# Optimization experiments

Hardware: AMD Instinct MI355X
Metric: run time of the kernel (lower is better)

Reference implementation:

```python
import jax, jax.numpy as jnp
import numpy as np

B, S, HID = 2, 2048, 2048
NK, NV, DK, DV, K = 16, 32, 128, 128, 4
KEY_DIM = NK * DK          # 2048
VAL_DIM = NV * DV          # 4096
CONV_DIM = 2 * KEY_DIM + VAL_DIM  # 8192
EPS = 1e-6


def setup_inputs() -> dict:
    key = jax.random.key(0)
    ks = jax.random.split(key, 8)
    n = lambda k, shape, sc: jax.random.normal(k, shape, jnp.float32) * sc
    return {
        "hidden_states": n(ks[0], (B, S, HID), 1.0),
        "W_qkv": n(ks[1], (CONV_DIM, HID), 0.02),
        "W_z": n(ks[2], (VAL_DIM, HID), 0.02),
        "W_b": n(ks[3], (NV, HID), 0.02),
        "W_a": n(ks[4], (NV, HID), 0.02),
        "conv_w": n(ks[5], (CONV_DIM, K), 0.3),   # depthwise conv weight, squeeze(1) of [C,1,K]
        "norm_w": jnp.ones((DV,), jnp.float32),
        "W_out": n(ks[6], (HID, VAL_DIM), 0.02),
        "dt_bias": jnp.ones((NV,), jnp.float32),
        "A_log": jnp.zeros((NV,), jnp.float32),
    }


def _l2norm(t):
    return t * jax.lax.rsqrt(jnp.sum(t * t, axis=-1, keepdims=True) + EPS)


def _forward(hidden_states, W_qkv, W_z, W_b, W_a, conv_w, norm_w, W_out, dt_bias, A_log):
    b_, s_, _ = hidden_states.shape
    mixed = hidden_states @ W_qkv.T                     # [B,S,CONV_DIM]
    z = (hidden_states @ W_z.T).reshape(b_, s_, NV, DV)  # gate branch
    b_proj = hidden_states @ W_b.T                      # [B,S,NV]
    a_proj = hidden_states @ W_a.T                      # [B,S,NV]

    # causal depthwise conv1d (groups=CONV_DIM, no bias) + silu
    x = jnp.transpose(mixed, (0, 2, 1))                 # [B,C,S]
    x = jnp.pad(x, ((0, 0), (0, 0), (K - 1, 0)))
    x = jax.lax.conv_general_dilated(
        x, conv_w[:, None, :], window_strides=(1,), padding="VALID",
        feature_group_count=CONV_DIM)
    mixed = jnp.transpose(jax.nn.silu(x), (0, 2, 1))    # [B,S,CONV_DIM]

    q, k, v = jnp.split(mixed, [KEY_DIM, 2 * KEY_DIM], axis=-1)
    q = q.reshape(b_, s_, NK, DK)
    k = k.reshape(b_, s_, NK, DK)
    v = v.reshape(b_, s_, NV, DV)

    beta = jax.nn.sigmoid(b_proj)                                    # [B,S,NV]
    g = -jnp.exp(A_log) * jax.nn.softplus(a_proj + dt_bias)          # [B,S,NV], log decay

    rep = NV // NK
    q = jnp.repeat(q, rep, axis=2)                      # GQA expand -> [B,S,NV,DK]
    k = jnp.repeat(k, rep, axis=2)
    q = _l2norm(q)
    k = _l2norm(k)
    scale = DK ** -0.5

    def step(state, inp):  # state: [B,NV,DK,DV]
        qt, kt, vt, gt, bt = inp  # [B,NV,DK],[B,NV,DK],[B,NV,DV],[B,NV],[B,NV]
        state = state * jnp.exp(gt)[..., None, None]
        mem = jnp.einsum('bhk,bhkv->bhv', kt, state)
        delta = (vt - mem) * bt[..., None]
        state = state + jnp.einsum('bhk,bhv->bhkv', kt, delta)
        ot = jnp.einsum('bhk,bhkv->bhv', qt * scale, state)
        return state, ot

    init = jnp.zeros((b_, NV, DK, DV), jnp.float32)
    xs = (jnp.moveaxis(q, 1, 0), jnp.moveaxis(k, 1, 0), jnp.moveaxis(v, 1, 0),
          jnp.moveaxis(g, 1, 0), jnp.moveaxis(beta, 1, 0))
    _, o = jax.lax.scan(step, init, xs)                 # [S,B,NV,DV]
    o = jnp.moveaxis(o, 0, 1)                           # [B,S,NV,DV]

    # RMSNormGated over head_v_dim, then silu(z) gate
    var = jnp.mean(o * o, axis=-1, keepdims=True)
    o = o * jax.lax.rsqrt(var + EPS) * norm_w
    o = (o * jax.nn.silu(z)).reshape(b_, s_, VAL_DIM)
    return o @ W_out.T


def reference(hidden_states, W_qkv, W_z, W_b, W_a, conv_w, norm_w, W_out, dt_bias, A_log):
    return _forward(hidden_states, W_qkv, W_z, W_b, W_a, conv_w, norm_w, W_out, dt_bias, A_log)
```

## Files before the change

kernel.cpp:

```cpp
#include <hip/hip_runtime.h>
#include <hip/hip_bf16.h>
#include <math.h>

#define DEVI __device__ __forceinline__

typedef __attribute__((ext_vector_type(4))) float f32x4;
typedef __attribute__((ext_vector_type(8))) short s16x8;
typedef __attribute__((ext_vector_type(4))) unsigned int u32x4;

DEVI float bf2f(ushort u){ union{unsigned int i; float f;} x; x.i = ((unsigned int)u)<<16; return x.f; }
DEVI ushort f2bf(float f){ union{float f; unsigned int i;} x; x.f = f;
  unsigned int r = x.i + 0x7fffu + ((x.i>>16)&1u); return (ushort)(r>>16); }

#define MFMA16(a,b,c) __builtin_amdgcn_mfma_f32_16x16x32_bf16(a,b,c,0,0,0)

__global__ __launch_bounds__(256) void cvt_bf16(const float* __restrict__ in, ushort* __restrict__ out){
  int i = blockIdx.x*256 + threadIdx.x;
  float4 v = ((const float4*)in)[i];
  ushort4 o; o.x = f2bf(v.x); o.y = f2bf(v.y); o.z = f2bf(v.z); o.w = f2bf(v.w);
  ((ushort4*)out)[i] = o;
}

DEVI void gl_lds16(const ushort* g, ushort* l){
  __builtin_amdgcn_global_load_lds((const __attribute__((address_space(1))) void*)g,
                                   (__attribute__((address_space(3))) void*)l, 16, 0, 0);
}

#define SBAR() __builtin_amdgcn_s_barrier()
#define LGKM0() do{ asm volatile("s_waitcnt lgkmcnt(0)" ::: "memory"); __builtin_amdgcn_sched_barrier(0); }while(0)
#define VMC6() asm volatile("s_waitcnt vmcnt(6)" ::: "memory")
#define VMC4() asm volatile("s_waitcnt vmcnt(4)" ::: "memory")

template<int BF16_OUT>
__global__ __launch_bounds__(512, 2) void gemm256(const ushort* __restrict__ A,
                                                  const ushort* __restrict__ B,
                                                  void* __restrict__ Cv,
                                                  int M, int N, int K,
                                                  int rpx, int cpx){
  __shared__ ushort smem[65536];
  __shared__ ushort dummy[4096];
  const int tid = threadIdx.x, w = tid>>6, lane = tid&63;
  const int fr = lane&15, quad = lane>>4;
  const int wm = w>>2, wn = w&3;
  const int NT = K>>6;

  const int nbn = N>>8;
  const int bid = blockIdx.x;
  const int xcd = bid & 7, idx = bid >> 3;
  const int CGn = nbn / cpx;
  const int rgrp = xcd / CGn, cgrp = xcd % CGn;
  const int rloc = idx % rpx, cloc = idx / rpx;
  const long tileM = (long)(rgrp*rpx + rloc) << 8;
  const long tileN = (long)(cgrp*cpx + cloc) << 8;

  const int rr  = (tid&63)>>2;
  const int cc  = ((tid&3)*8) ^ ((rr&8)?16:0);
  const int row0 = (w>>1)*16 + rr;
  const int col0 = (w&1)*32 + cc;
  const long off0 = (long)row0*K + col0;
  const long h64 = 64l*K;

  const ushort* pA0 = A + tileM*K + off0;
  const ushort* pA1 = pA0 + 128l*K;
  const ushort* pB0 = B + tileN*K + off0;
  const ushort* pB1 = pB0 + 128l*K;

  const int dw = w*512;
  ushort* dmy = dummy + dw;

#define ST_A0(bb,tt) do{ if((tt)<NT){ const long kk=(long)(tt)<<6; \
    gl_lds16(pA0+kk, smem+(bb)*32768+dw);        gl_lds16(pA1+kk, smem+(bb)*32768+8192+dw);} \
    else { gl_lds16(pA0, dmy); gl_lds16(pA1, dmy);} }while(0)
#define ST_A1(bb,tt) do{ if((tt)<NT){ const long kk=((long)(tt)<<6)+h64; \
    gl_lds16(pA0+kk, smem+(bb)*32768+4096+dw);   gl_lds16(pA1+kk, smem+(bb)*32768+12288+dw);} \
    else { gl_lds16(pA0, dmy); gl_lds16(pA1, dmy);} }while(0)
#define ST_B0(bb,tt) do{ if((tt)<NT){ const long kk=(long)(tt)<<6; \
    gl_lds16(pB0+kk, smem+(bb)*32768+16384+dw);  gl_lds16(pB1+kk, smem+(bb)*32768+24576+dw);} \
    else { gl_lds16(pB0, dmy); gl_lds16(pB1, dmy);} }while(0)
#define ST_B1(bb,tt) do{ if((tt)<NT){ const long kk=((long)(tt)<<6)+h64; \
    gl_lds16(pB0+kk, smem+(bb)*32768+20480+dw);  gl_lds16(pB1+kk, smem+(bb)*32768+28672+dw);} \
    else { gl_lds16(pB0, dmy); gl_lds16(pB1, dmy);} }while(0)

  const int baseF = fr*32 + ((quad*8) ^ ((fr&8)?16:0));
  const int sB = (wn&1)*4;

  f32x4 acc[8][4];
  #pragma unroll
  for (int i=0;i<8;i++)
    #pragma unroll
    for (int j=0;j<4;j++) acc[i][j] = (f32x4){0.f,0.f,0.f,0.f};

  ST_A0(0,0); ST_B0(0,0); ST_B1(0,0); ST_A1(0,0);
  ST_A0(1,1); ST_B0(1,1); ST_B1(1,1);
  VMC6();
  SBAR();

  #pragma unroll 2
  for (int t=0; t<NT; ++t){
    const int bs = t&1;
    const ushort* SA = smem + bs*32768 + wm*8192;
    const ushort* SB = smem + bs*32768 + 16384 + (wn>>1)*8192;
    s16x8 af[4][2], bl[2][2], bh[2][2];
    #pragma unroll
    for (int mt=0;mt<4;mt++)
      #pragma unroll
      for (int ks=0;ks<2;ks++)
        af[mt][ks] = *(const s16x8*)(SA + ((mt*2+ks)<<9) + baseF);
    #pragma unroll
    for (int nt=0;nt<2;nt++)
      #pragma unroll
      for (int ks=0;ks<2;ks++)
        bl[nt][ks] = *(const s16x8*)(SB + (((sB+nt)*2+ks)<<9) + baseF);
    ST_A1(bs^1, t+1);
    SBAR(); LGKM0();
    __builtin_amdgcn_s_setprio(1);
    #pragma unroll
    for (int mt=0;mt<4;mt++)
      #pragma unroll
      for (int nt=0;nt<2;nt++){
        acc[mt][nt] = MFMA16(af[mt][0], bl[nt][0], acc[mt][nt]);
        acc[mt][nt] = MFMA16(af[mt][1], bl[nt][1], acc[mt][nt]);
      }
    __builtin_amdgcn_s_setprio(0);
    SBAR();
    #pragma unroll
    for (int nt=0;nt<2;nt++)
      #pragma unroll
      for (int ks=0;ks<2;ks++)
        bh[nt][ks] = *(const s16x8*)(SB + (((sB+2+nt)*2+ks)<<9) + baseF);
    ST_A0(bs, t+2);
    SBAR(); LGKM0();
    __builtin_amdgcn_s_setprio(1);
    #pragma unroll
    for (int mt=0;mt<4;mt++)
      #pragma unroll
      for (int nt=0;nt<2;nt++){
        acc[mt][2+nt] = MFMA16(af[mt][0], bh[nt][0], acc[mt][2+nt]);
        acc[mt][2+nt] = MFMA16(af[mt][1], bh[nt][1], acc[mt][2+nt]);
      }
    __builtin_amdgcn_s_setprio(0);
    SBAR();
    #pragma unroll
    for (int mt=0;mt<4;mt++)
      #pragma unroll
      for (int ks=0;ks<2;ks++)
        af[mt][ks] = *(const s16x8*)(SA + (((4+mt)*2+ks)<<9) + baseF);
    ST_B0(bs, t+2);
    SBAR(); LGKM0();
    __builtin_amdgcn_s_setprio(1);
    #pragma unroll
    for (int mt=0;mt<4;mt++)
      #pragma unroll
      for (int nt=0;nt<2;nt++){
        acc[4+mt][nt] = MFMA16(af[mt][0], bl[nt][0], acc[4+mt][nt]);
        acc[4+mt][nt] = MFMA16(af[mt][1], bl[nt][1], acc[4+mt][nt]);
      }
    __builtin_amdgcn_s_setprio(0);
    SBAR();
    ST_B1(bs, t+2);
    SBAR();
    __builtin_amdgcn_s_setprio(1);
    #pragma unroll
    for (int mt=0;mt<4;mt++)
      #pragma unroll
      for (int nt=0;nt<2;nt++){
        acc[4+mt][2+nt] = MFMA16(af[mt][0], bh[nt][0], acc[4+mt][2+nt]);
        acc[4+mt][2+nt] = MFMA16(af[mt][1], bh[nt][1], acc[4+mt][2+nt]);
      }
    __builtin_amdgcn_s_setprio(0);
    VMC6();
    SBAR();
  }
#undef ST_A0
#undef ST_A1
#undef ST_B0
#undef ST_B1

  const long Rb = tileM + wm*128 + quad*4;
  const long Cb = tileN + wn*64 + fr;
  if (BF16_OUT){
    ushort* C = (ushort*)Cv;
    #pragma unroll
    for (int mt=0;mt<8;mt++)
      #pragma unroll
      for (int r=0;r<4;r++){
        const long row = Rb + mt*16 + r;
        #pragma unroll
        for (int nt=0;nt<4;nt++)
          C[row*(long)N + Cb + nt*16] = f2bf(acc[mt][nt][r]);
      }
  } else {
    float* C = (float*)Cv;
    #pragma unroll
    for (int mt=0;mt<8;mt++)
      #pragma unroll
      for (int r=0;r<4;r++){
        const long row = Rb + mt*16 + r;
        #pragma unroll
        for (int nt=0;nt<4;nt++)
          C[row*(long)N + Cb + nt*16] = acc[mt][nt][r];
      }
  }
}

template<int BF16_OUT>
__global__ __launch_bounds__(512, 2) void gemm256n128(const ushort* __restrict__ A,
                                                      const ushort* __restrict__ B,
                                                      void* __restrict__ Cv,
                                                      int M, int N, int K,
                                                      int rpx, int cpx){
  __shared__ ushort smem[49152];
  __shared__ ushort dummy[4096];
  const int tid = threadIdx.x, w = tid>>6, lane = tid&63;
  const int fr = lane&15, quad = lane>>4;
  const int wm = w>>2, wn = w&3;
  const int NT = K>>6;

  const int nbn = N>>7;
  const int bid = blockIdx.x;
  const int xcd = bid & 7, idx = bid >> 3;
  const int CGn = nbn / cpx;
  const int rgrp = xcd / CGn, cgrp = xcd % CGn;
  const int rloc = idx % rpx, cloc = idx / rpx;
  const long tileM = (long)(rgrp*rpx + rloc) << 8;
  const long tileN = (long)(cgrp*cpx + cloc) << 7;

  const int rr  = (tid&63)>>2;
  const int cc  = ((tid&3)*8) ^ ((rr&8)?16:0);
  const int row0 = (w>>1)*16 + rr;
  const int col0 = (w&1)*32 + cc;
  const long off0 = (long)row0*K + col0;
  const long h64 = 64l*K;

  const ushort* pA0 = A + tileM*K + off0;
  const ushort* pA1 = pA0 + 128l*K;
  const ushort* pB0 = B + tileN*K + off0;

  const int dw = w*512;
  ushort* dmy = dummy + dw;

#define ST_A0(bb,tt) do{ if((tt)<NT){ const long kk=(long)(tt)<<6; \
    gl_lds16(pA0+kk, smem+(bb)*24576+dw);        gl_lds16(pA1+kk, smem+(bb)*24576+8192+dw);} \
    else { gl_lds16(pA0, dmy); gl_lds16(pA1, dmy);} }while(0)
#define ST_A1(bb,tt) do{ if((tt)<NT){ const long kk=((long)(tt)<<6)+h64; \
    gl_lds16(pA0+kk, smem+(bb)*24576+4096+dw);   gl_lds16(pA1+kk, smem+(bb)*24576+12288+dw);} \
    else { gl_lds16(pA0, dmy); gl_lds16(pA1, dmy);} }while(0)
#define ST_B(bb,tt) do{ if((tt)<NT){ const long kk=(long)(tt)<<6; \
    gl_lds16(pB0+kk, smem+(bb)*24576+16384+dw);  gl_lds16(pB0+kk+h64, smem+(bb)*24576+20480+dw);} \
    else { gl_lds16(pB0, dmy); gl_lds16(pB0, dmy);} }while(0)

  const int baseF = fr*32 + ((quad*8) ^ ((fr&8)?16:0));

  f32x4 acc[8][2];
  #pragma unroll
  for (int i=0;i<8;i++)
    #pragma unroll
    for (int j=0;j<2;j++) acc[i][j] = (f32x4){0.f,0.f,0.f,0.f};

  ST_A0(0,0); ST_B(0,0); ST_A1(0,0);
  ST_A0(1,1); ST_B(1,1);
  VMC4();
  SBAR();

  #pragma unroll 2
  for (int t=0; t<NT; ++t){
    const int bs = t&1;
    const ushort* SA = smem + bs*24576 + wm*8192;
    const ushort* SB = smem + bs*24576 + 16384;
    s16x8 af[4][2], bl[2], bh[2];
    #pragma unroll
    for (int mt=0;mt<4;mt++)
      #pragma unroll
      for (int ks=0;ks<2;ks++)
        af[mt][ks] = *(const s16x8*)(SA + ((mt*2+ks)<<9) + baseF);
    #pragma unroll
    for (int ks=0;ks<2;ks++)
      bl[ks] = *(const s16x8*)(SB + (((wn*2+0)*2+ks)<<9) + baseF);
    ST_A1(bs^1, t+1);
    SBAR(); LGKM0();
    __builtin_amdgcn_s_setprio(1);
    #pragma unroll
    for (int mt=0;mt<4;mt++){
      acc[mt][0] = MFMA16(af[mt][0], bl[0], acc[mt][0]);
      acc[mt][0] = MFMA16(af[mt][1], bl[1], acc[mt][0]);
    }
    __builtin_amdgcn_s_setprio(0);
    SBAR();
    #pragma unroll
    for (int ks=0;ks<2;ks++)
      bh[ks] = *(const s16x8*)(SB + (((wn*2+1)*2+ks)<<9) + baseF);
    ST_A0(bs, t+2);
    SBAR(); LGKM0();
    __builtin_amdgcn_s_setprio(1);
    #pragma unroll
    for (int mt=0;mt<4;mt++){
      acc[mt][1] = MFMA16(af[mt][0], bh[0], acc[mt][1]);
      acc[mt][1] = MFMA16(af[mt][1], bh[1], acc[mt][1]);
    }
    __builtin_amdgcn_s_setprio(0);
    SBAR();
    #pragma unroll
    for (int mt=0;mt<4;mt++)
      #pragma unroll
      for (int ks=0;ks<2;ks++)
        af[mt][ks] = *(const s16x8*)(SA + (((4+mt)*2+ks)<<9) + baseF);
    ST_B(bs, t+2);
    SBAR(); LGKM0();
    __builtin_amdgcn_s_setprio(1);
    #pragma unroll
    for (int mt=0;mt<4;mt++){
      acc[4+mt][0] = MFMA16(af[mt][0], bl[0], acc[4+mt][0]);
      acc[4+mt][0] = MFMA16(af[mt][1], bl[1], acc[4+mt][0]);
    }
    __builtin_amdgcn_s_setprio(0);
    SBAR();
    __builtin_amdgcn_s_setprio(1);
    #pragma unroll
    for (int mt=0;mt<4;mt++){
      acc[4+mt][1] = MFMA16(af[mt][0], bh[0], acc[4+mt][1]);
      acc[4+mt][1] = MFMA16(af[mt][1], bh[1], acc[4+mt][1]);
    }
    __builtin_amdgcn_s_setprio(0);
    VMC4();
    SBAR();
  }
#undef ST_A0
#undef ST_A1
#undef ST_B

  const long Rb = tileM + wm*128 + quad*4;
  const long Cb = tileN + wn*32 + fr;
  if (BF16_OUT){
    ushort* C = (ushort*)Cv;
    #pragma unroll
    for (int mt=0;mt<8;mt++)
      #pragma unroll
      for (int r=0;r<4;r++){
        const long row = Rb + mt*16 + r;
        #pragma unroll
        for (int nt=0;nt<2;nt++)
          C[row*(long)N + Cb + nt*16] = f2bf(acc[mt][nt][r]);
      }
  } else {
    float* C = (float*)Cv;
    #pragma unroll
    for (int mt=0;mt<8;mt++)
      #pragma unroll
      for (int r=0;r<4;r++){
        const long row = Rb + mt*16 + r;
        #pragma unroll
        for (int nt=0;nt<2;nt++)
          C[row*(long)N + Cb + nt*16] = acc[mt][nt][r];
      }
  }
}

__global__ __launch_bounds__(256, 2) void gemm_ba(const ushort* __restrict__ A,
                                                  const ushort* __restrict__ B,
                                                  float* __restrict__ Cp){
  __shared__ ushort As[128*32];
  __shared__ ushort Bs[128*32];
  const int mt0 = blockIdx.x>>3, ks = blockIdx.x&7;
  const int tile_m = mt0<<7;
  const int tid  = threadIdx.x;
  const int w    = tid >> 6;
  const int lane = tid & 63;
  const int K = 2048;

  const int ca = w*2;
  const long rowA = tile_m + ca*16 + (lane>>2);
  const long rowB = ca*16 + (lane>>2);
  const int  colE = (lane&3)*8 + ks*256;
  const ushort* pA0 = A + rowA*(long)K + colE;
  const ushort* pA1 = pA0 + 16l*K;
  const ushort* pB0 = B + rowB*(long)K + colE;
  const ushort* pB1 = pB0 + 16l*K;
  ushort* lA0 = As + ca*512;
  ushort* lA1 = As + ca*512 + 512;
  ushort* lB0 = Bs + ca*512;
  ushort* lB1 = Bs + ca*512 + 512;

  const int wr = (w>>1)<<6;
  const int wc = (w&1)<<6;
  const int fr = lane & 15;
  const int fk = (lane>>4)<<3;

  f32x4 acc[4][4];
  #pragma unroll
  for (int i=0;i<4;i++)
    #pragma unroll
    for (int j=0;j<4;j++) acc[i][j] = (f32x4){0.f,0.f,0.f,0.f};

  for (int k0 = 0; k0 < 256; k0 += 32){
    __syncthreads();
    gl_lds16(pA0, lA0);
    gl_lds16(pA1, lA1);
    gl_lds16(pB0, lB0);
    gl_lds16(pB1, lB1);
    __syncthreads();
    s16x8 af[4], bfr[4];
    #pragma unroll
    for (int t=0;t<4;t++){
      af[t]  = *(const s16x8*)(As + (wr + t*16 + fr)*32 + fk);
      bfr[t] = *(const s16x8*)(Bs + (wc + t*16 + fr)*32 + fk);
    }
    #pragma unroll
    for (int mt=0;mt<4;mt++)
      #pragma unroll
      for (int nt=0;nt<4;nt++)
        acc[mt][nt] = MFMA16(af[mt], bfr[nt], acc[mt][nt]);
    pA0 += 32; pA1 += 32; pB0 += 32; pB1 += 32;
  }

  float* C = Cp + (long)ks*524288;
  const int crow = tile_m + wr + ((lane>>4)<<2);
  const int ccol = wc + (lane&15);
  #pragma unroll
  for (int mt=0;mt<4;mt++)
    #pragma unroll
    for (int r=0;r<4;r++){
      long row = crow + mt*16 + r;
      #pragma unroll
      for (int nt=0;nt<4;nt++)
        C[row*128 + ccol + nt*16] = acc[mt][nt][r];
    }
}

__global__ __launch_bounds__(256) void ba_post2(const float* __restrict__ bp,
    const float* __restrict__ dtb, const float* __restrict__ alog,
    float* __restrict__ beta, float* __restrict__ glog){
  const int idx = blockIdx.x*256 + threadIdx.x;
  const int m = idx >> 6, j = idx & 63;
  float v = 0.f;
  #pragma unroll
  for (int s=0;s<8;s++) v += bp[(long)s*524288 + (long)m*128 + j];
  if (j < 32){
    beta[(long)m*32 + j] = 1.f/(1.f+expf(-v));
  } else {
    const int n = j - 32;
    float ap = v + dtb[n];
    float sp = (ap > 20.f) ? ap : log1pf(expf(ap));
    glog[(long)m*32 + n] = -expf(alog[n]) * sp;
  }
}

__global__ __launch_bounds__(256) void conv_qkv2(const ushort* __restrict__ mixed,
    const float* __restrict__ convw, ushort* __restrict__ qn, ushort* __restrict__ kn,
    ushort* __restrict__ vv){
  const long m0 = (long)blockIdx.x * 32;
  const int ct = blockIdx.y;
  const int ch = (ct<<11) + threadIdx.x*8;
  const ushort* base = mixed + ch;

  ushort* outp; int mode; float qsc = 1.f;
  if (ct == 0){ outp = qn + ch;        mode = 0; qsc = 0.08838834764831845f; }
  else if (ct == 1){ outp = kn + (ch-2048); mode = 1; }
  else { outp = vv + (ch-4096); mode = 2; }

  float cw0[8], cw1[8], cw2[8], cw3[8];
  #pragma unroll
  for (int e=0;e<8;e++){
    float4 wv = *(const float4*)(convw + (long)(ch+e)*4);
    cw0[e]=wv.x; cw1[e]=wv.y; cw2[e]=wv.z; cw3[e]=wv.w;
  }

#define LDROW(PTR, R) do{ s16x8 _v = *(const s16x8*)(PTR); \
    _Pragma("unroll") \
    for (int e=0;e<8;e++) R[e] = bf2f((ushort)_v[e]); }while(0)

#define STEP(P0,P1,P2,P3,MR) do{ \
    float y[8]; float ss = 0.f; \
    _Pragma("unroll") \
    for (int e=0;e<8;e++){ \
      float a = P0[e]*cw0[e]; \
      a += P1[e]*cw1[e]; \
      a += P2[e]*cw2[e]; \
      a += P3[e]*cw3[e]; \
      float sv = a / (1.f + expf(-a)); \
      y[e] = sv; ss += sv*sv; } \
    if (mode < 2){ \
      ss += __shfl_xor(ss,1); ss += __shfl_xor(ss,2); \
      ss += __shfl_xor(ss,4); ss += __shfl_xor(ss,8); \
      const float r_ = rsqrtf(ss + 1e-6f) * qsc; \
      s16x8 ov; \
      _Pragma("unroll") \
      for (int e=0;e<8;e++) ov[e] = (short)f2bf(y[e]*r_); \
      *(s16x8*)(outp + (MR)*2048) = ov; \
    } else { \
      s16x8 ov; \
      _Pragma("unroll") \
      for (int e=0;e<8;e++) ov[e] = (short)f2bf(y[e]); \
      *(s16x8*)(outp + (MR)*4096) = ov; \
    } \
  }while(0)

  float w3[8], w2[8], w1[8];
  if (((int)m0 & 2047) == 0){
    #pragma unroll
    for (int e=0;e<8;e++){ w3[e]=0.f; w2[e]=0.f; w1[e]=0.f; }
  } else {
    LDROW(base + (m0-3)*8192, w3);
    LDROW(base + (m0-2)*8192, w2);
    LDROW(base + (m0-1)*8192, w1);
  }

  long m = m0;
  for (int it=0; it<8; ++it){
    float r0[8], r1[8], r2[8], r3[8];
    LDROW(base + (m+0)*8192, r0);
    LDROW(base + (m+1)*8192, r1);
    LDROW(base + (m+2)*8192, r2);
    LDROW(base + (m+3)*8192, r3);
    STEP(w3,w2,w1,r0, m+0);
    STEP(w2,w1,r0,r1, m+1);
    STEP(w1,r0,r1,r2, m+2);
    STEP(r0,r1,r2,r3, m+3);
    #pragma unroll
    for (int e=0;e<8;e++){ w3[e]=r1[e]; w2[e]=r2[e]; w1[e]=r3[e]; }
    m += 4;
  }
#undef LDROW
#undef STEP
}

__global__ __launch_bounds__(256) void chunk_prep(
    const ushort* __restrict__ qn, const ushort* __restrict__ kn,
    const float* __restrict__ beta, const float* __restrict__ glog,
    ushort* __restrict__ Tg, ushort* __restrict__ Mg, float* __restrict__ cumLgG){
  const int bid = blockIdx.x;
  const int bh = bid >> 6, ch = bid & 63;
  const int b = bh>>5, h = bh&31, hq = h>>1;
  const long tch = (long)b*2048 + ch*32;
  const int tid = threadIdx.x, w = tid>>6, lane = tid&63;
  const int quad = lane>>4, l15 = lane&15;

  __shared__ __attribute__((aligned(16))) ushort Kl[32][136];
  __shared__ __attribute__((aligned(16))) ushort Ql[32][136];
  __shared__ float Asl[32][33];
  __shared__ float Lgl[32], Btl[32];

  const int sc = tid>>3, ss = (tid&7)*16;
  {
    const ushort* kp = kn + (tch+sc)*2048 + hq*128 + ss;
    const ushort* qp = qn + (tch+sc)*2048 + hq*128 + ss;
    *(u32x4*)&Kl[sc][ss] = *(const u32x4*)kp; *(u32x4*)&Kl[sc][ss+8] = *(const u32x4*)(kp+8);
    *(u32x4*)&Ql[sc][ss] = *(const u32x4*)qp; *(u32x4*)&Ql[sc][ss+8] = *(const u32x4*)(qp+8);
  }
  if (tid < 64){
    const int c = lane & 31;
    float gv = glog[(tch + c)*32 + h];
    float bv = beta[(tch + c)*32 + h];
    #pragma unroll
    for (int off=1; off<32; off<<=1){
      float t = __shfl_up(gv, off);
      if ((lane & 31) >= off) gv += t;
    }
    if (lane < 32){ Lgl[c] = gv; Btl[c] = bv; cumLgG[(long)bid*32 + c] = gv; }
  }
  __syncthreads();

  const int mt = w>>1, nt = w&1;
  s16x8 ka[4], qa[4], kb[4];
  #pragma unroll
  for (int ks=0; ks<4; ks++){
    ka[ks] = *(const s16x8*)&Kl[mt*16+l15][ks*32 + quad*8];
    qa[ks] = *(const s16x8*)&Ql[mt*16+l15][ks*32 + quad*8];
    kb[ks] = *(const s16x8*)&Kl[nt*16+l15][ks*32 + quad*8];
  }
  f32x4 accK = (f32x4){0.f,0.f,0.f,0.f}, accQ = (f32x4){0.f,0.f,0.f,0.f};
  #pragma unroll
  for (int ks=0; ks<4; ks++){
    accK = MFMA16(ka[ks], kb[ks], accK);
    accQ = MFMA16(qa[ks], kb[ks], accQ);
  }
  const int j = nt*16 + l15;
  const float Lgj = Lgl[j];
  #pragma unroll
  for (int i=0;i<4;i++){
    const int r = mt*16 + quad*4 + i;
    const float e = expf(Lgl[r]-Lgj);
    Asl[r][j] = (r>j) ? -Btl[r]*e*accK[i] : 0.f;
    Mg[(long)bid*1024 + r*32 + j] = (r>=j) ? f2bf(e*accQ[i]) : (ushort)0;
  }
  __syncthreads();

  if (tid < 32){
    const int jc = tid;
    float tc[32];
    #pragma unroll
    for (int c=0;c<32;c++){
      float acc = (c==jc) ? 1.f : 0.f;
      #pragma unroll
      for (int i2=0;i2<c;i2++) acc = fmaf(Asl[c][i2], tc[i2], acc);
      tc[c] = acc;
      Tg[(long)bid*1024 + c*32 + jc] = f2bf(acc);
    }
  }
}

__global__ __launch_bounds__(256, 2) void chunk_scan3(
    const ushort* __restrict__ qn, const ushort* __restrict__ kn,
    const ushort* __restrict__ vv, const float* __restrict__ beta,
    const float* __restrict__ cumLg, const ushort* __restrict__ Tg,
    const ushort* __restrict__ Mg, float* __restrict__ o){
  const int bh = blockIdx.x & 63, sl = blockIdx.x >> 6;
  const int b = bh>>5, h = bh&31, hq = h>>1;
  const int dv0 = sl<<4;
  const int tid = threadIdx.x, w = tid>>6, lane = tid&63;
  const int quad = lane>>4, l15 = lane&15;
  const int rt = w&1, kq = w>>1;

  __shared__ __attribute__((aligned(16))) ushort STl[16][136];
  __shared__ __attribute__((aligned(16))) ushort B0T[16][40];
  __shared__ __attribute__((aligned(16))) ushort DT[16][40];
  __shared__ float Btf[32], eLgl[32], eDf[32];

  const ushort* pKQ = (kq ? qn : kn) + ((long)b*2048 + rt*16 + l15)*2048 + hq*128 + quad*8;
  const ushort* pKT = kn + ((long)b*2048 + quad*8)*2048 + hq*128 + w*32 + l15;
  const ushort* pV  = vv + ((long)b*2048 + rt*16 + quad*4)*4096 + h*128 + dv0 + l15;
  const ushort* pTM = (kq ? Mg : Tg) + (long)bh*65536 + (rt*16 + l15)*32 + quad*8;
  const long pbBase = (long)bh*2048 + tid;
  const float* betaP = beta + ((long)b*2048 + tid)*32 + h;

  s16x8 cKQ[4], nKQ[4], cK0, cK1, nK0, nK1, cTM, nTM;
  ushort cV0=0,cV1=0,cV2=0,cV3=0, nV0=0,nV1=0,nV2=0,nV3=0;
  float cLg = 0.f, nLg = 0.f, cBt = 0.f, nBt = 0.f;

  f32x4 S0 = (f32x4){0.f,0.f,0.f,0.f}, S1 = (f32x4){0.f,0.f,0.f,0.f};

#define LOADCH(PKQ,PK0,PK1,PV0,PV1,PV2,PV3,PTMv,PLG,PBT,CH) do{ \
    const long co = (long)(CH)*65536; \
    _Pragma("unroll") \
    for (int ks=0; ks<4; ks++) PKQ[ks] = *(const s16x8*)(pKQ + co + ks*32); \
    _Pragma("unroll") \
    for (int e=0; e<8; e++){ \
      PK0[e] = (short)pKT[co + (long)e*2048]; \
      PK1[e] = (short)pKT[co + (long)e*2048 + 16]; } \
    if (kq == 0){ \
      const long vo = (long)(CH)*131072; \
      PV0 = pV[vo]; PV1 = pV[vo+4096]; PV2 = pV[vo+8192]; PV3 = pV[vo+12288]; } \
    PTMv = *(const s16x8*)(pTM + (long)(CH)*1024); \
    if (tid < 32){ PLG = cumLg[pbBase + (long)(CH)*32]; PBT = betaP[(long)(CH)*1024]; } \
  }while(0)

  LOADCH(cKQ, cK0, cK1, cV0,cV1,cV2,cV3, cTM, cLg, cBt, 0);

  for (int ch=0; ch<64; ch++){
    const long tch = (long)b*2048 + ch*32;
    LOADCH(nKQ, nK0, nK1, nV0,nV1,nV2,nV3, nTM, nLg, nBt, (ch<63)?(ch+1):63);
    if (tid < 32){
      float lgC = __shfl(cLg, 31);
      Btf[tid] = cBt;
      eLgl[tid] = expf(cLg);
      eDf[tid]  = expf(lgC - cLg);
    }
    {
      ushort4 p0, p1;
      p0.x=f2bf(S0[0]); p0.y=f2bf(S0[1]); p0.z=f2bf(S0[2]); p0.w=f2bf(S0[3]);
      p1.x=f2bf(S1[0]); p1.y=f2bf(S1[1]); p1.z=f2bf(S1[2]); p1.w=f2bf(S1[3]);
      *(ushort4*)&STl[l15][w*32 + quad*4]      = p0;
      *(ushort4*)&STl[l15][w*32 + 16 + quad*4] = p1;
    }
    __syncthreads();
    f32x4 acc = (f32x4){0.f,0.f,0.f,0.f};
    #pragma unroll
    for (int ks=0; ks<4; ks++){
      s16x8 sb = *(const s16x8*)&STl[l15][ks*32 + quad*8];
      acc = MFMA16(cKQ[ks], sb, acc);
    }
    if (kq == 0){
      const int c0r = rt*16 + quad*4;
      ushort4 pb;
      pb.x = f2bf(Btf[c0r+0]*(bf2f(cV0) - eLgl[c0r+0]*acc[0]));
      pb.y = f2bf(Btf[c0r+1]*(bf2f(cV1) - eLgl[c0r+1]*acc[1]));
      pb.z = f2bf(Btf[c0r+2]*(bf2f(cV2) - eLgl[c0r+2]*acc[2]));
      pb.w = f2bf(Btf[c0r+3]*(bf2f(cV3) - eLgl[c0r+3]*acc[3]));
      *(ushort4*)&B0T[l15][rt*16 + quad*4] = pb;
    } else {
      #pragma unroll
      for (int i=0;i<4;i++) acc[i] *= eLgl[rt*16 + quad*4 + i];
    }
    __syncthreads();
    const float eC = eLgl[31];
    s16x8 kta0, kta1;
    #pragma unroll
    for (int e=0;e<8;e++){
      const float ed = eDf[quad*8 + e];
      kta0[e] = (short)f2bf(bf2f((ushort)cK0[e])*ed);
      kta1[e] = (short)f2bf(bf2f((ushort)cK1[e])*ed);
    }
    if (kq == 0){
      s16x8 a = *(const s16x8*)&B0T[l15][quad*8];
      f32x4 Dt = MFMA16(a, cTM, ((f32x4){0.f,0.f,0.f,0.f}));
      #pragma unroll
      for (int i=0;i<4;i++)
        DT[quad*4+i][rt*16 + l15] = f2bf(Dt[i]);
    }
    __syncthreads();
    s16x8 df = *(const s16x8*)&DT[l15][quad*8];
    if (kq == 1){
      f32x4 O = MFMA16(cTM, df, acc);
      #pragma unroll
      for (int i=0;i<4;i++)
        o[(tch + rt*16 + quad*4 + i)*4096 + h*128 + dv0 + l15] = O[i];
    }
    f32x4 t0, t1;
    #pragma unroll
    for (int i=0;i<4;i++){ t0[i] = S0[i]*eC; t1[i] = S1[i]*eC; }
    S0 = MFMA16(kta0, df, t0);
    S1 = MFMA16(kta1, df, t1);
    #pragma unroll
    for (int ks=0; ks<4; ks++) cKQ[ks] = nKQ[ks];
    cK0 = nK0; cK1 = nK1; cTM = nTM;
    cV0 = nV0; cV1 = nV1; cV2 = nV2; cV3 = nV3;
    cLg = nLg; cBt = nBt;
  }
#undef LOADCH
}

__global__ __launch_bounds__(256) void norm_gate2(const float* __restrict__ o,
    const ushort* __restrict__ z, const float* __restrict__ normw,
    ushort* __restrict__ og){
  const int tid = threadIdx.x;
  const int rg = tid>>5, l = tid&31;
  const int d0 = l*4;
  const float4 nw = *(const float4*)(normw + d0);
  long row = (long)blockIdx.x*32 + rg;
  #pragma unroll
  for (int it=0; it<4; ++it){
    const float4 xv = *(const float4*)(o + row*128 + d0);
    const ushort4 zv = *(const ushort4*)(z + row*128 + d0);
    float ss = xv.x*xv.x + xv.y*xv.y + xv.z*xv.z + xv.w*xv.w;
    ss += __shfl_xor(ss,1); ss += __shfl_xor(ss,2); ss += __shfl_xor(ss,4);
    ss += __shfl_xor(ss,8); ss += __shfl_xor(ss,16);
    const float r = rsqrtf(ss*(1.f/128.f) + 1e-6f);
    ushort4 ov; float zz, sil;
    zz = bf2f(zv.x); sil = zz/(1.f+expf(-zz)); ov.x = f2bf(xv.x*r*nw.x*sil);
    zz = bf2f(zv.y); sil = zz/(1.f+expf(-zz)); ov.y = f2bf(xv.y*r*nw.y*sil);
    zz = bf2f(zv.z); sil = zz/(1.f+expf(-zz)); ov.z = f2bf(xv.z*r*nw.z*sil);
    zz = bf2f(zv.w); sil = zz/(1.f+expf(-zz)); ov.w = f2bf(xv.w*r*nw.w*sil);
    *(ushort4*)(og + row*128 + d0) = ov;
    row += 8;
  }
}

extern "C" void kernel_launch(void* const* d_in, const int* in_sizes, int n_in,
                              void* d_out, int out_size, void* d_ws, size_t ws_size,
                              hipStream_t stream){
  const float* hs    = (const float*)d_in[0];
  const float* Wqkv  = (const float*)d_in[1];
  const float* Wz    = (const float*)d_in[2];
  const float* Wb    = (const float*)d_in[3];
  const float* Wa    = (const float*)d_in[4];
  const float* convw = (const float*)d_in[5];
  const float* normw = (const float*)d_in[6];
  const float* Wout  = (const float*)d_in[7];
  const float* dtb   = (const float*)d_in[8];
  const float* alog  = (const float*)d_in[9];

  char* ws = (char*)d_ws;
  ushort* hsb   = (ushort*)(ws);
  ushort* wqb   = (ushort*)(ws + (16l<<20));
  ushort* wzb   = (ushort*)(ws + (48l<<20));
  ushort* wob   = (ushort*)(ws + (64l<<20));
  ushort* mixed = (ushort*)(ws + (80l<<20));
  ushort* zb    = (ushort*)(ws + (144l<<20));
  float*  beta  = (float*)(ws + (176l<<20));
  float*  cumLg = (float*)(ws + (176l<<20) + (512l<<10));
  float*  glog  = (float*)(ws + (177l<<20));
  ushort* Tg    = (ushort*)(ws + (178l<<20));
  ushort* Mg    = (ushort*)(ws + (186l<<20));
  ushort* wbab  = (ushort*)(ws + (194l<<20));
  float*  bapr8 = (float*)(ws + (178l<<20));
  ushort* kn = hsb;  ushort* qn = wzb;  ushort* vvp = wqb;  ushort* og = wqb;
  float*  o_raw = (float*)mixed;

  cvt_bf16<<<8192,  256, 0, stream>>>(hs,   hsb);
  cvt_bf16<<<16384, 256, 0, stream>>>(Wqkv, wqb);
  cvt_bf16<<<8192,  256, 0, stream>>>(Wz,   wzb);
  cvt_bf16<<<8192,  256, 0, stream>>>(Wout, wob);
  cvt_bf16<<<64,    256, 0, stream>>>(Wb,   wbab);
  cvt_bf16<<<64,    256, 0, stream>>>(Wa,   wbab + 65536);

  gemm256<1><<<512, 512, 0, stream>>>(hsb, wqb, (void*)mixed, 4096, 8192, 2048, 4, 16);
  gemm256<1><<<256, 512, 0, stream>>>(hsb, wzb, (void*)zb,    4096, 4096, 2048, 4, 8);
  gemm_ba<<<256, 256, 0, stream>>>(hsb, wbab, bapr8);
  ba_post2<<<1024, 256, 0, stream>>>(bapr8, dtb, alog, beta, glog);

  conv_qkv2<<<dim3(128,4), 256, 0, stream>>>(mixed, convw, qn, kn, vvp);
  chunk_prep<<<4096, 256, 0, stream>>>(qn, kn, beta, glog, Tg, Mg, cumLg);
  chunk_scan3<<<512, 256, 0, stream>>>(qn, kn, vvp, beta, cumLg, Tg, Mg, o_raw);
  norm_gate2<<<4096, 256, 0, stream>>>(o_raw, zb, normw, og);

  gemm256n128<0><<<256, 512, 0, stream>>>(og, wob, d_out, 4096, 2048, 4096, 4, 8);
}
```

Measured before the change: 655.6 us.

## Simplify GEMM main loop to plain double-buffered single-stage pipeline

Replaces the finely interleaved four-phase GEMM loop, which staged partial A/B sub-tiles two iterations ahead and kept several barriers per iteration, with a simple double-buffered loop. Each iteration loads all fragments from LDS, issues the full next-tile global-to-LDS copy, runs all MFMAs, then waits for vmcnt(0) and synchronises once. This drops the dummy-buffer loads and most barriers, but shortens prefetch depth and raises register pressure from holding all fragments at once, which may expose memory latency.

```diff
diff --git a/kernel.cpp b/kernel.cpp
--- a/kernel.cpp
+++ b/kernel.cpp
@@ -28,7 +28,7 @@
 
 #define SBAR() __builtin_amdgcn_s_barrier()
 #define LGKM0() do{ asm volatile("s_waitcnt lgkmcnt(0)" ::: "memory"); __builtin_amdgcn_sched_barrier(0); }while(0)
-#define VMC6() asm volatile("s_waitcnt vmcnt(6)" ::: "memory")
+#define VMC0() asm volatile("s_waitcnt vmcnt(0)" ::: "memory")
 #define VMC4() asm volatile("s_waitcnt vmcnt(4)" ::: "memory")
 
 template<int BF16_OUT>
@@ -38,7 +38,6 @@
                                                   int M, int N, int K,
                                                   int rpx, int cpx){
   __shared__ ushort smem[65536];
-  __shared__ ushort dummy[4096];
   const int tid = threadIdx.x, w = tid>>6, lane = tid&63;
   const int fr = lane&15, quad = lane>>4;
   const int wm = w>>2, wn = w&3;
@@ -66,20 +65,16 @@
   const ushort* pB1 = pB0 + 128l*K;
 
   const int dw = w*512;
-  ushort* dmy = dummy + dw;
-
-#define ST_A0(bb,tt) do{ if((tt)<NT){ const long kk=(long)(tt)<<6; \
-    gl_lds16(pA0+kk, smem+(bb)*32768+dw);        gl_lds16(pA1+kk, smem+(bb)*32768+8192+dw);} \
-    else { gl_lds16(pA0, dmy); gl_lds16(pA1, dmy);} }while(0)
-#define ST_A1(bb,tt) do{ if((tt)<NT){ const long kk=((long)(tt)<<6)+h64; \
-    gl_lds16(pA0+kk, smem+(bb)*32768+4096+dw);   gl_lds16(pA1+kk, smem+(bb)*32768+12288+dw);} \
-    else { gl_lds16(pA0, dmy); gl_lds16(pA1, dmy);} }while(0)
-#define ST_B0(bb,tt) do{ if((tt)<NT){ const long kk=(long)(tt)<<6; \
-    gl_lds16(pB0+kk, smem+(bb)*32768+16384+dw);  gl_lds16(pB1+kk, smem+(bb)*32768+24576+dw);} \
-    else { gl_lds16(pB0, dmy); gl_lds16(pB1, dmy);} }while(0)
-#define ST_B1(bb,tt) do{ if((tt)<NT){ const long kk=((long)(tt)<<6)+h64; \
-    gl_lds16(pB0+kk, smem+(bb)*32768+20480+dw);  gl_lds16(pB1+kk, smem+(bb)*32768+28672+dw);} \
-    else { gl_lds16(pB0, dmy); gl_lds16(pB1, dmy);} }while(0)
+
+#define STG(bb,tt) do{ if((tt)<NT){ const long kk=(long)(tt)<<6; \
+    gl_lds16(pA0+kk,     smem+(bb)*32768+dw); \
+    gl_lds16(pA0+kk+h64, smem+(bb)*32768+4096+dw); \
+    gl_lds16(pA1+kk,     smem+(bb)*32768+8192+dw); \
+    gl_lds16(pA1+kk+h64, smem+(bb)*32768+12288+dw); \
+    gl_lds16(pB0+kk,     smem+(bb)*32768+16384+dw); \
+    gl_lds16(pB0+kk+h64, smem+(bb)*32768+20480+dw); \
+    gl_lds16(pB1+kk,     smem+(bb)*32768+24576+dw); \
+    gl_lds16(pB1+kk+h64, smem+(bb)*32768+28672+dw); } }while(0)
 
   const int baseF = fr*32 + ((quad*8) ^ ((fr&8)?16:0));
   const int sB = (wn&1)*4;
@@ -90,91 +85,39 @@
     #pragma unroll
     for (int j=0;j<4;j++) acc[i][j] = (f32x4){0.f,0.f,0.f,0.f};
 
-  ST_A0(0,0); ST_B0(0,0); ST_B1(0,0); ST_A1(0,0);
-  ST_A0(1,1); ST_B0(1,1); ST_B1(1,1);
-  VMC6();
+  STG(0,0);
+  VMC0();
   SBAR();
-
-  #pragma unroll 2
+  __builtin_amdgcn_sched_barrier(0);
+
   for (int t=0; t<NT; ++t){
     const int bs = t&1;
     const ushort* SA = smem + bs*32768 + wm*8192;
     const ushort* SB = smem + bs*32768 + 16384 + (wn>>1)*8192;
-    s16x8 af[4][2], bl[2][2], bh[2][2];
-    #pragma unroll
-    for (int mt=0;mt<4;mt++)
-      #pragma unroll
-      for (int ks=0;ks<2;ks++)
-        af[mt][ks] = *(const s16x8*)(SA + ((mt*2+ks)<<9) + baseF);
-    #pragma unroll
-    for (int nt=0;nt<2;nt++)
-      #pragma unroll
-      for (int ks=0;ks<2;ks++)
-        bl[nt][ks] = *(const s16x8*)(SB + (((sB+nt)*2+ks)<<9) + baseF);
-    ST_A1(bs^1, t+1);
-    SBAR(); LGKM0();
+    s16x8 af[8][2], bf[4][2];
+    #pragma unroll
+    for (int nt=0;nt<4;nt++) bf[nt][0] = *(const s16x8*)(SB + (((sB+nt)*2+0)<<9) + baseF);
+    #pragma unroll
+    for (int mt=0;mt<8;mt++) af[mt][0] = *(const s16x8*)(SA + ((mt*2+0)<<9) + baseF);
+    #pragma unroll
+    for (int nt=0;nt<4;nt++) bf[nt][1] = *(const s16x8*)(SB + (((sB+nt)*2+1)<<9) + baseF);
+    #pragma unroll
+    for (int mt=0;mt<8;mt++) af[mt][1] = *(const s16x8*)(SA + ((mt*2+1)<<9) + baseF);
+    STG(bs^1, t+1);
     __builtin_amdgcn_s_setprio(1);
     #pragma unroll
-    for (int mt=0;mt<4;mt++)
-      #pragma unroll
-      for (int nt=0;nt<2;nt++){
-        acc[mt][nt] = MFMA16(af[mt][0], bl[nt][0], acc[mt][nt]);
-        acc[mt][nt] = MFMA16(af[mt][1], bl[nt][1], acc[mt][nt]);
-      }
+    for (int ks=0;ks<2;ks++)
+      #pragma unroll
+      for (int mt=0;mt<8;mt++)
+        #pragma unroll
+        for (int nt=0;nt<4;nt++)
+          acc[mt][nt] = MFMA16(af[mt][ks], bf[nt][ks], acc[mt][nt]);
     __builtin_amdgcn_s_setprio(0);
+    VMC0();
     SBAR();
-    #pragma unroll
-    for (int nt=0;nt<2;nt++)
-      #pragma unroll
-      for (int ks=0;ks<2;ks++)
-        bh[nt][ks] = *(const s16x8*)(SB + (((sB+2+nt)*2+ks)<<9) + baseF);
-    ST_A0(bs, t+2);
-    SBAR(); LGKM0();
-    __builtin_amdgcn_s_setprio(1);
-    #pragma unroll
-    for (int mt=0;mt<4;mt++)
-      #pragma unroll
-      for (int nt=0;nt<2;nt++){
-        acc[mt][2+nt] = MFMA16(af[mt][0], bh[nt][0], acc[mt][2+nt]);
-        acc[mt][2+nt] = MFMA16(af[mt][1], bh[nt][1], acc[mt][2+nt]);
-      }
-    __builtin_amdgcn_s_setprio(0);
-    SBAR();
-    #pragma unroll
-    for (int mt=0;mt<4;mt++)
-      #pragma unroll
-      for (int ks=0;ks<2;ks++)
-        af[mt][ks] = *(const s16x8*)(SA + (((4+mt)*2+ks)<<9) + baseF);
-    ST_B0(bs, t+2);
-    SBAR(); LGKM0();
-    __builtin_amdgcn_s_setprio(1);
-    #pragma unroll
-    for (int mt=0;mt<4;mt++)
-      #pragma unroll
-      for (int nt=0;nt<2;nt++){
-        acc[4+mt][nt] = MFMA16(af[mt][0], bl[nt][0], acc[4+mt][nt]);
-        acc[4+mt][nt] = MFMA16(af[mt][1], bl[nt][1], acc[4+mt][nt]);
-      }
-    __builtin_amdgcn_s_setprio(0);
-    SBAR();
-    ST_B1(bs, t+2);
-    SBAR();
-    __builtin_amdgcn_s_setprio(1);
-    #pragma unroll
-    for (int mt=0;mt<4;mt++)
-      #pragma unroll
-      for (int nt=0;nt<2;nt++){
-        acc[4+mt][2+nt] = MFMA16(af[mt][0], bh[nt][0], acc[4+mt][2+nt]);
-        acc[4+mt][2+nt] = MFMA16(af[mt][1], bh[nt][1], acc[4+mt][2+nt]);
-      }
-    __builtin_amdgcn_s_setprio(0);
-    VMC6();
-    SBAR();
-  }
-#undef ST_A0
-#undef ST_A1
-#undef ST_B0
-#undef ST_B1
+    __builtin_amdgcn_sched_barrier(0);
+  }
+#undef STG
 
   const long Rb = tileM + wm*128 + quad*4;
   const long Cb = tileN + wn*64 + fr;
```

Result: no change. 653.4 us (-0.3%).
